# Optimization experiments

Measured on AMD Instinct MI355X. Metric: run time of the kernel, lower is better.

## Reference

```python
import jax, jax.numpy as jnp
import numpy as np

EPS = 1e-12


def conv3(x, W, b):
    # x: [B,C,H,W], W: [O,I,3,3] -> SAME conv, stride 1
    y = jax.lax.conv_general_dilated(x, W, (1, 1), 'SAME',
                                     dimension_numbers=('NCHW', 'OIHW', 'NCHW'))
    return y + b[None, :, None, None]


def unfold3(x):
    # torch F.unfold(kernel=3, padding=1): [B,C,H,W] -> [B, C*9, H*W]
    B, C, H, W = x.shape
    xp = jnp.pad(x, ((0, 0), (0, 0), (1, 1), (1, 1)))
    patches = jnp.stack([xp[:, :, i:i + H, j:j + W]
                         for i in range(3) for j in range(3)], axis=2)  # [B,C,9,H,W]
    return patches.reshape(B, C * 9, H * W)


def fold3(u, H, W):
    # torch F.fold(kernel=3, padding=1): [B, C*9, H*W] -> [B,C,H,W] (overlap-add)
    B = u.shape[0]
    C = u.shape[1] // 9
    p = u.reshape(B, C, 3, 3, H, W)
    out = jnp.zeros((B, C, H + 2, W + 2), u.dtype)
    for i in range(3):
        for j in range(3):
            out = out.at[:, :, i:i + H, j:j + W].add(p[:, :, i, j])
    return out[:, :, 1:-1, 1:-1]


def l2norm(v, axis):
    n = jnp.sqrt(jnp.sum(v * v, axis=axis, keepdims=True))
    return v / jnp.maximum(n, EPS)


def setup_inputs() -> dict:
    key = jax.random.key(0)
    ks = jax.random.split(key, 10)
    in_c, q_c = 64, 32
    B, H, W = 1, 96, 96
    s = 0.05
    return {
        'x':  jax.random.normal(ks[0], (B, in_c, H, W), jnp.float32),
        'W1': jax.random.normal(ks[1], (in_c, in_c, 3, 3), jnp.float32) * s,
        'b1': jax.random.normal(ks[2], (in_c,), jnp.float32) * s,
        'W2': jax.random.normal(ks[3], (in_c, in_c, 3, 3), jnp.float32) * s,
        'b2': jax.random.normal(ks[4], (in_c,), jnp.float32) * s,
        'Wq': jax.random.normal(ks[5], (q_c, in_c, 3, 3), jnp.float32) * s,
        'bq': jax.random.normal(ks[6], (q_c,), jnp.float32) * s,
        'Wk': jax.random.normal(ks[7], (q_c, in_c, 3, 3), jnp.float32) * s,
        'bk': jax.random.normal(ks[8], (q_c,), jnp.float32) * s,
    }


def reference(x, W1, b1, W2, b2, Wq, bq, Wk, bk):
    TOPK = 5
    B, C, H, W = x.shape
    L = H * W

    feature = jax.nn.relu(conv3(jax.nn.relu(conv3(x, W1, b1)), W2, b2))
    q = conv3(x, Wq, bq)
    k = conv3(x, Wk, bk)

    q_unfold = l2norm(unfold3(q), axis=1)                      # [B, Q9, L]
    k_unfold = l2norm(jnp.swapaxes(unfold3(k), 1, 2), axis=2)  # [B, L, Q9]

    R_qk = jnp.einsum('blc,bcm->blm', k_unfold, q_unfold)      # [B, L_k, L_q]

    # topk over dim=1 (key positions) for each query position
    vals, idxs = jax.lax.top_k(jnp.swapaxes(R_qk, 1, 2), TOPK)  # [B, L_q, K]
    R_maxs = jnp.swapaxes(vals, 1, 2)                           # [B, K, L]
    R_indexs = jnp.swapaxes(idxs, 1, 2)                         # [B, K, L]

    x_unfold = unfold3(x)                                       # [B, C*9, L]
    acc = jnp.zeros_like(x)
    for i in range(1, TOPK):
        idx = R_indexs[:, i, :][:, None, :]                     # [B,1,L]
        T_unfold = jnp.take_along_axis(x_unfold, idx, axis=2)   # [B, C*9, L]
        T = fold3(T_unfold, H, W) / 9.0
        S = R_maxs[:, i, :].reshape(B, 1, H, W)
        acc = acc + T * S
    y = feature + x + acc / float(TOPK - 1)
    return y
```

## Files before the change

### kernel.cpp

```cpp
#include <hip/hip_runtime.h>
#include <math.h>

#define HH 96
#define WW 96
#define LL 9216
#define PW 98
#define PCH (PW * PW)
#define D9 288
#define TOPK 5
#define NK 6
#define NCAND 8
#define KSPLIT 32
#define CPQ (KSPLIT * NK)
#define KEYS_PER_SPLIT (LL / KSPLIT)
#define PASSES (KEYS_PER_SPLIT / 32)
#define CHUNKS (32 * 36)
#define KROW 292

typedef short short8 __attribute__((ext_vector_type(8)));
typedef float f32x16 __attribute__((ext_vector_type(16)));

__device__ __forceinline__ float  asf(unsigned u) { union { unsigned u; float f; } a; a.u = u; return a.f; }
__device__ __forceinline__ unsigned asu(float f)  { union { float f; unsigned u; } a; a.f = f; return a.u; }

__device__ __forceinline__ unsigned short f2bf(float f) {
    unsigned u = asu(f);
    unsigned r = u + 0x7fff + ((u >> 16) & 1);
    return (unsigned short)(r >> 16);
}

template<int N>
__device__ __forceinline__ void ins_med3(float* v, float x) {
    float nv[N];
    nv[0] = fmaxf(v[0], x);
    #pragma unroll
    for (int s = 1; s < N; ++s) nv[s] = __builtin_amdgcn_fmed3f(v[s-1], v[s], x);
    #pragma unroll
    for (int s = 0; s < N; ++s) v[s] = nv[s];
}

__device__ __forceinline__ bool better_tb(float av, int ai, float bv, int bi) {
    return (av > bv) || (av == bv && ai < bi);
}

template<int N>
__device__ __forceinline__ void insert_tb(float (&v)[N], int (&ix)[N], float nv, int ni) {
    if (better_tb(nv, ni, v[N-1], ix[N-1])) {
        v[N-1] = nv; ix[N-1] = ni;
        #pragma unroll
        for (int s = N-1; s > 0; --s) {
            if (better_tb(v[s], ix[s], v[s-1], ix[s-1])) {
                float tv = v[s]; v[s] = v[s-1]; v[s-1] = tv;
                int ti = ix[s]; ix[s] = ix[s-1]; ix[s-1] = ti;
            }
        }
    }
}

__global__ __launch_bounds__(256) void pad_init_kernel(
    const float* __restrict__ x, float* __restrict__ xpad, float* __restrict__ c1pad)
{
    int e = blockIdx.x * 256 + threadIdx.x;
    if (blockIdx.y == 1) { c1pad[e] = 0.0f; return; }
    int c = e / PCH, rem = e - c * PCH;
    int r = rem / PW, col = rem - r * PW;
    float val = 0.0f;
    if ((unsigned)(r - 1) < 96u && (unsigned)(col - 1) < 96u)
        val = x[(size_t)c * LL + (r - 1) * WW + (col - 1)];
    xpad[e] = val;
}

template<int NCO>
__device__ __forceinline__ void conv_pipe(
    const float* __restrict__ inpad, const float* __restrict__ Wt,
    const float* __restrict__ bias, int co0,
    float (&acc)[NCO][2])
{
    int t = blockIdx.x * 256 + threadIdx.x;
    int pix0 = t * 2;
    int y = pix0 / WW, x0 = pix0 - y * WW;
    const float* base = inpad + y * PW + x0;

    #pragma unroll
    for (int j = 0; j < NCO; ++j) acc[j][0] = acc[j][1] = bias[co0 + j];

    float2 A[3][2], B[3][2];
    #pragma unroll
    for (int u = 0; u < 3; ++u) {
        A[u][0] = *(const float2*)(base + u * PW);
        A[u][1] = *(const float2*)(base + u * PW + 2);
    }

    #pragma unroll 1
    for (int ci = 0; ci < 64; ci += 2) {
        const float* nb = base + (size_t)(ci + 1) * PCH;
        #pragma unroll
        for (int u = 0; u < 3; ++u) {
            B[u][0] = *(const float2*)(nb + u * PW);
            B[u][1] = *(const float2*)(nb + u * PW + 2);
        }
        {
            const float* wb = Wt + ((size_t)co0 * 64 + ci) * 9;
            #pragma unroll
            for (int j = 0; j < NCO; ++j) {
                const float* wp = wb + (size_t)j * 64 * 9;
                #pragma unroll
                for (int u = 0; u < 3; ++u) {
                    float r0 = A[u][0].x, r1 = A[u][0].y, r2 = A[u][1].x, r3 = A[u][1].y;
                    float w0 = wp[u*3], w1 = wp[u*3+1], w2 = wp[u*3+2];
                    acc[j][0] = fmaf(r0, w0, acc[j][0]);
                    acc[j][1] = fmaf(r1, w0, acc[j][1]);
                    acc[j][0] = fmaf(r1, w1, acc[j][0]);
                    acc[j][1] = fmaf(r2, w1, acc[j][1]);
                    acc[j][0] = fmaf(r2, w2, acc[j][0]);
                    acc[j][1] = fmaf(r3, w2, acc[j][1]);
                }
            }
        }
        if (ci + 2 < 64) {
            const float* nb2 = base + (size_t)(ci + 2) * PCH;
            #pragma unroll
            for (int u = 0; u < 3; ++u) {
                A[u][0] = *(const float2*)(nb2 + u * PW);
                A[u][1] = *(const float2*)(nb2 + u * PW + 2);
            }
        }
        {
            const float* wb = Wt + ((size_t)co0 * 64 + (ci + 1)) * 9;
            #pragma unroll
            for (int j = 0; j < NCO; ++j) {
                const float* wp = wb + (size_t)j * 64 * 9;
                #pragma unroll
                for (int u = 0; u < 3; ++u) {
                    float r0 = B[u][0].x, r1 = B[u][0].y, r2 = B[u][1].x, r3 = B[u][1].y;
                    float w0 = wp[u*3], w1 = wp[u*3+1], w2 = wp[u*3+2];
                    acc[j][0] = fmaf(r0, w0, acc[j][0]);
                    acc[j][1] = fmaf(r1, w0, acc[j][1]);
                    acc[j][0] = fmaf(r1, w1, acc[j][0]);
                    acc[j][1] = fmaf(r2, w1, acc[j][1]);
                    acc[j][0] = fmaf(r2, w2, acc[j][0]);
                    acc[j][1] = fmaf(r3, w2, acc[j][1]);
                }
            }
        }
    }
}

__global__ __launch_bounds__(256) void conv_stage1_kernel(
    const float* __restrict__ xpad,
    const float* __restrict__ W1, const float* __restrict__ b1, float* __restrict__ c1pad,
    const float* __restrict__ Wq, const float* __restrict__ bq,
    const float* __restrict__ Wk, const float* __restrict__ bk,
    float* __restrict__ qq, float* __restrict__ kk)
{
    int g = blockIdx.y;
    int pix0 = (blockIdx.x * 256 + threadIdx.x) * 2;
    int y = pix0 / WW, x0 = pix0 - y * WW;

    if (g < 16) {
        float acc[4][2];
        conv_pipe<4>(xpad, W1, b1, g * 4, acc);
        #pragma unroll
        for (int j = 0; j < 4; ++j) {
            float* o = c1pad + (size_t)(g * 4 + j) * PCH + (y + 1) * PW + (x0 + 1);
            o[0] = fmaxf(acc[j][0], 0.0f);
            o[1] = fmaxf(acc[j][1], 0.0f);
        }
    } else if (g < 24) {
        float acc[4][2];
        conv_pipe<4>(xpad, Wq, bq, (g - 16) * 4, acc);
        #pragma unroll
        for (int j = 0; j < 4; ++j)
            *(float2*)(qq + (size_t)((g - 16) * 4 + j) * LL + pix0) = make_float2(acc[j][0], acc[j][1]);
    } else {
        float acc[4][2];
        conv_pipe<4>(xpad, Wk, bk, (g - 24) * 4, acc);
        #pragma unroll
        for (int j = 0; j < 4; ++j)
            *(float2*)(kk + (size_t)((g - 24) * 4 + j) * LL + pix0) = make_float2(acc[j][0], acc[j][1]);
    }
}

__global__ __launch_bounds__(256) void conv2_kernel(
    const float* __restrict__ c1pad, const float* __restrict__ W2,
    const float* __restrict__ b2, float* __restrict__ feat)
{
    int pix0 = (blockIdx.x * 256 + threadIdx.x) * 2;
    float acc[2][2];
    conv_pipe<2>(c1pad, W2, b2, blockIdx.y * 2, acc);
    #pragma unroll
    for (int j = 0; j < 2; ++j) {
        float2 o;
        o.x = fmaxf(acc[j][0], 0.0f);
        o.y = fmaxf(acc[j][1], 0.0f);
        *(float2*)(feat + (size_t)(blockIdx.y * 2 + j) * LL + pix0) = o;
    }
}

__global__ __launch_bounds__(256) void transpose_x_kernel(
    const float* __restrict__ x, float* __restrict__ xT)
{
    __shared__ float t[64][65];
    int pix0 = blockIdx.x * 64;
    int lp = threadIdx.x & 63, cg = threadIdx.x >> 6;
    #pragma unroll
    for (int cc = 0; cc < 16; ++cc) {
        int c = cg * 16 + cc;
        t[c][lp] = x[(size_t)c * LL + pix0 + lp];
    }
    __syncthreads();
    #pragma unroll
    for (int pp = 0; pp < 16; ++pp) {
        int pl = cg * 16 + pp;
        xT[(size_t)(pix0 + pl) * 64 + lp] = t[lp][pl];
    }
}

__global__ __launch_bounds__(256) void unfold_norm_kernel(
    const float* __restrict__ qq, float* __restrict__ q_f32, unsigned short* __restrict__ q_bf,
    const float* __restrict__ kk, float* __restrict__ k_f32, unsigned short* __restrict__ k_bf)
{
    const float* in; float* o32; unsigned short* obf;
    if (blockIdx.y == 0) { in = qq; o32 = q_f32; obf = q_bf; }
    else                 { in = kk; o32 = k_f32; obf = k_bf; }

    __shared__ float tile[3][32][34];
    __shared__ float inv_s[32];
    int tid = threadIdx.x;
    int l0 = blockIdx.x * 32;
    int y = l0 / WW, xb = l0 % WW;

    #pragma unroll
    for (int j = 0; j < 13; ++j) {
        int f = j * 256 + tid;
        if (f < 3 * 32 * 34) {
            int col = f % 34, cc = (f / 34) & 31, r = f / (34 * 32);
            int yy = y + r - 1, xv = xb + col - 1;
            float val = ((unsigned)yy < 96u && (unsigned)xv < 96u)
                        ? in[(size_t)cc * LL + yy * 96 + xv] : 0.0f;
            tile[r][cc][col] = val;
        }
    }
    __syncthreads();

    {
        int pxl = tid >> 3, sub = tid & 7;
        float ss = 0.0f;
        #pragma unroll
        for (int cc = 0; cc < 4; ++cc) {
            int c = sub * 4 + cc;
            #pragma unroll
            for (int u = 0; u < 3; ++u)
                #pragma unroll
                for (int v = 0; v < 3; ++v) {
                    float val = tile[u][c][pxl + v];
                    ss = fmaf(val, val, ss);
                }
        }
        ss += __shfl_xor(ss, 1);
        ss += __shfl_xor(ss, 2);
        ss += __shfl_xor(ss, 4);
        if (sub == 0) inv_s[pxl] = 1.0f / fmaxf(sqrtf(ss), 1e-12f);
    }
    __syncthreads();

    #pragma unroll 1
    for (int it = 0; it < 9; ++it) {
        int e = it * 256 + tid;
        int pxl = e / 72, dc = e - pxl * 72;
        int l = l0 + pxl;
        float inv = inv_s[pxl];
        float4 o; float* op = &o.x;
        #pragma unroll
        for (int i = 0; i < 4; ++i) {
            int d = dc * 4 + i;
            int c = d / 9, rm = d - c * 9;
            int u = rm / 3, v = rm - u * 3;
            op[i] = tile[u][c][pxl + v] * inv;
        }
        *(float4*)(o32 + (size_t)l * D9 + dc * 4) = o;
        unsigned short b4[4];
        #pragma unroll
        for (int i = 0; i < 4; ++i) b4[i] = f2bf(op[i]);
        *(uint2*)(obf + (size_t)l * D9 + dc * 4) = *(uint2*)b4;
    }
}

__global__ __launch_bounds__(256, 2) void topk_mfma_kernel(
    const unsigned short* __restrict__ qn_bf, const unsigned short* __restrict__ kn_bf,
    float* __restrict__ valsQ)
{
    __shared__ unsigned short ks[2][32 * KROW];

    int tid  = threadIdx.x;
    int lane = tid & 63;
    int col = lane & 31, khalf = lane >> 5;
    int qtile = blockIdx.x >> 5;
    int split = blockIdx.x & 31;
    int q0w = qtile * 256 + (tid >> 6) * 64;
    int key0 = split * KEYS_PER_SPLIT;

    short8 qf[2][18];
    #pragma unroll
    for (int b = 0; b < 2; ++b) {
        const unsigned short* qrow = qn_bf + (size_t)(q0w + b*32 + col) * D9 + khalf * 8;
        #pragma unroll
        for (int dg = 0; dg < 18; ++dg)
            qf[b][dg] = *(const short8*)(qrow + dg * 16);
    }

    float lv0[NK], lv1[NK];
    #pragma unroll
    for (int s = 0; s < NK; ++s) { lv0[s] = -INFINITY; lv1[s] = -INFINITY; }

    const char* kg = (const char*)kn_bf;
    uint4 pre[5];

    #pragma unroll
    for (int c0 = 0; c0 < 5; ++c0) {
        int c = tid + c0 * 256;
        if (c < CHUNKS) {
            int key = c / 36, off = c - key * 36;
            pre[c0] = *(const uint4*)(kg + (size_t)(key0 + key) * 576 + off * 16);
        }
    }
    #pragma unroll
    for (int c0 = 0; c0 < 5; ++c0) {
        int c = tid + c0 * 256;
        if (c < CHUNKS) {
            int key = c / 36, off = c - key * 36;
            char* d = (char*)ks[0] + key * (KROW*2) + off * 16;
            *(uint2*)d       = *(uint2*)&pre[c0];
            *(uint2*)(d + 8) = *((uint2*)&pre[c0] + 1);
        }
    }
    __syncthreads();

    for (int p = 0; p < PASSES; ++p) {
        if (p + 1 < PASSES) {
            #pragma unroll
            for (int c0 = 0; c0 < 5; ++c0) {
                int c = tid + c0 * 256;
                if (c < CHUNKS) {
                    int key = c / 36, off = c - key * 36;
                    pre[c0] = *(const uint4*)(kg + (size_t)(key0 + (p+1)*32 + key) * 576 + off * 16);
                }
            }
        }

        f32x16 acc0 = {}, acc1 = {};
        const char* kb = (const char*)ks[p & 1] + (size_t)col * (KROW*2) + khalf * 16;
        #pragma unroll
        for (int dg = 0; dg < 18; ++dg) {
            short8 af;
            *(uint2*)&af       = *(const uint2*)(kb + dg * 32);
            *((uint2*)&af + 1) = *(const uint2*)(kb + dg * 32 + 8);
            acc0 = __builtin_amdgcn_mfma_f32_32x32x16_bf16(af, qf[0][dg], acc0, 0, 0, 0);
            acc1 = __builtin_amdgcn_mfma_f32_32x32x16_bf16(af, qf[1][dg], acc1, 0, 0, 0);
        }

        int lbase = p * 32 + 4 * khalf;
        #pragma unroll
        for (int r = 0; r < 16; ++r) {
            unsigned lkey = (unsigned)(lbase + (r & 3) + 8 * (r >> 2));
            ins_med3<NK>(lv0, asf((asu(acc0[r]) & 0xFFFFFE00u) | lkey));
            ins_med3<NK>(lv1, asf((asu(acc1[r]) & 0xFFFFFE00u) | lkey));
        }

        if (p + 1 < PASSES) {
            #pragma unroll
            for (int c0 = 0; c0 < 5; ++c0) {
                int c = tid + c0 * 256;
                if (c < CHUNKS) {
                    int key = c / 36, off = c - key * 36;
                    char* d = (char*)ks[(p+1) & 1] + key * (KROW*2) + off * 16;
                    *(uint2*)d       = *(uint2*)&pre[c0];
                    *(uint2*)(d + 8) = *((uint2*)&pre[c0] + 1);
                }
            }
        }
        __syncthreads();
    }

    #pragma unroll
    for (int b = 0; b < 2; ++b) {
        float* lv = b ? lv1 : lv0;
        float pv[NK];
        #pragma unroll
        for (int s = 0; s < NK; ++s) pv[s] = __shfl_xor(lv[s], 32);
        #pragma unroll
        for (int s = 0; s < NK; ++s) ins_med3<NK>(lv, pv[s]);
        if (lane < 32) {
            int q = q0w + b * 32 + col;
            float* vq = valsQ + (size_t)q * CPQ + split * NK;
            #pragma unroll
            for (int s = 0; s < NK; ++s) vq[s] = lv[s];
        }
    }
}

__global__ __launch_bounds__(256) void rerank_kernel(
    const float* __restrict__ valsQ,
    const float* __restrict__ qn_f32, const float* __restrict__ kn_f32,
    float* __restrict__ vals, int* __restrict__ idxs)
{
    int tid = threadIdx.x;
    int lane = tid & 63;
    int half = lane >> 5, l32 = lane & 31;
    int q = blockIdx.x * 8 + (tid >> 6) * 2 + half;

    const float* vq = valsQ + (size_t)q * CPQ + l32 * NK;
    float v[NK];
    #pragma unroll
    for (int s = 0; s < NK; ++s) v[s] = vq[s];

    int ckey[NCAND];
    #pragma unroll
    for (int it = 0; it < NCAND; ++it) {
        float cv = v[0];
        int cl = l32;
        #pragma unroll
        for (int st = 1; st < 32; st <<= 1) {
            float ov = __shfl_xor(cv, st);
            int ol = __shfl_xor(cl, st);
            if (ov > cv || (ov == cv && ol < cl)) { cv = ov; cl = ol; }
        }
        ckey[it] = cl * KEYS_PER_SPLIT + (int)(asu(cv) & 0x1FFu);
        if (cl == l32) {
            #pragma unroll
            for (int s = 0; s < NK-1; ++s) v[s] = v[s+1];
            v[NK-1] = -INFINITY;
        }
    }

    int r = l32 >> 2, part = l32 & 3;
    const float4* qr = (const float4*)(qn_f32 + (size_t)q * D9) + part * 18;
    const float4* kr = (const float4*)(kn_f32 + (size_t)ckey[r] * D9) + part * 18;
    float s0 = 0.f, s1 = 0.f, s2 = 0.f, s3 = 0.f;
    #pragma unroll
    for (int i2 = 0; i2 < 18; ++i2) {
        float4 a = qr[i2], b = kr[i2];
        s0 = fmaf(a.x, b.x, s0); s1 = fmaf(a.y, b.y, s1);
        s2 = fmaf(a.z, b.z, s2); s3 = fmaf(a.w, b.w, s3);
    }
    float sc = (s0 + s1) + (s2 + s3);
    sc += __shfl_xor(sc, 1);
    sc += __shfl_xor(sc, 2);

    float bv[TOPK]; int bi[TOPK];
    #pragma unroll
    for (int s = 0; s < TOPK; ++s) { bv[s] = -INFINITY; bi[s] = 0x7fffffff; }
    #pragma unroll
    for (int cc = 0; cc < NCAND; ++cc) {
        float sv = __shfl(sc, half * 32 + cc * 4);
        insert_tb<TOPK>(bv, bi, sv, ckey[cc]);
    }
    if (l32 == 0) {
        #pragma unroll
        for (int s = 0; s < TOPK; ++s) {
            vals[(size_t)s * LL + q] = bv[s];
            idxs[(size_t)s * LL + q] = bi[s];
        }
    }
}

__global__ __launch_bounds__(256) void gather_out_kernel(
    const float* __restrict__ xT, const float* __restrict__ feat,
    const float* __restrict__ vals, const int* __restrict__ idxs,
    float* __restrict__ out)
{
    int wave = threadIdx.x >> 6, lane = threadIdx.x & 63;
    int pix = blockIdx.x * 4 + wave;
    int y = pix / WW, x0 = pix - y * WW;
    float acc = 0.0f;
    #pragma unroll 1
    for (int s = 1; s < TOPK; ++s) {
        float S = vals[(size_t)s * LL + pix] * (1.0f/9.0f);
        #pragma unroll
        for (int i = 0; i < 3; ++i) {
            int qy = y + 1 - i;
            #pragma unroll
            for (int j = 0; j < 3; ++j) {
                int qx = x0 + 1 - j;
                if ((unsigned)qy < 96u && (unsigned)qx < 96u) {
                    int l = idxs[(size_t)s * LL + qy * WW + qx];
                    int yl = l / WW, xl = l - yl * WW;
                    int sy = yl + i - 1, sx = xl + j - 1;
                    if ((unsigned)sy < 96u && (unsigned)sx < 96u)
                        acc = fmaf(S, xT[(size_t)(sy * WW + sx) * 64 + lane], acc);
                }
            }
        }
    }
    out[(size_t)lane * LL + pix] = feat[(size_t)lane * LL + pix]
                                 + xT[(size_t)pix * 64 + lane] + acc * 0.25f;
}

extern "C" void kernel_launch(void* const* d_in, const int* in_sizes, int n_in,
                              void* d_out, int out_size, void* d_ws, size_t ws_size,
                              hipStream_t stream)
{
    (void)in_sizes; (void)n_in; (void)out_size; (void)ws_size;
    const float* x  = (const float*)d_in[0];
    const float* W1 = (const float*)d_in[1];
    const float* b1 = (const float*)d_in[2];
    const float* W2 = (const float*)d_in[3];
    const float* b2 = (const float*)d_in[4];
    const float* Wq = (const float*)d_in[5];
    const float* bq = (const float*)d_in[6];
    const float* Wk = (const float*)d_in[7];
    const float* bk = (const float*)d_in[8];
    float* out = (float*)d_out;

    char* p = (char*)d_ws;
    float* xpad   = (float*)p;            p += (size_t)64 * PCH * 4;
    float* c1pad  = (float*)p;            p += (size_t)64 * PCH * 4;
    float* feat   = (float*)p;            p += (size_t)64 * LL * 4;
    float* xT     = (float*)p;            p += (size_t)64 * LL * 4;
    float* qq     = (float*)p;            p += (size_t)32 * LL * 4;
    float* kk     = (float*)p;            p += (size_t)32 * LL * 4;
    float* qn_f32 = (float*)p;            p += (size_t)LL * D9 * 4;
    float* kn_f32 = (float*)p;            p += (size_t)LL * D9 * 4;
    unsigned short* qn_bf = (unsigned short*)p;  p += (size_t)LL * D9 * 2;
    unsigned short* kn_bf = (unsigned short*)p;  p += (size_t)LL * D9 * 2;
    float* valsQ  = (float*)p;            p += (size_t)LL * CPQ * 4;
    float* vals   = (float*)p;            p += (size_t)TOPK * LL * 4;
    int*   idxs   = (int*)p;              p += (size_t)TOPK * LL * 4;

    pad_init_kernel<<<dim3(2401, 2), 256, 0, stream>>>(x, xpad, c1pad);
    conv_stage1_kernel<<<dim3(18, 32), 256, 0, stream>>>(xpad, W1, b1, c1pad, Wq, bq, Wk, bk, qq, kk);
    unfold_norm_kernel<<<dim3(288, 2), 256, 0, stream>>>(qq, qn_f32, qn_bf, kk, kn_f32, kn_bf);
    topk_mfma_kernel<<<36 * KSPLIT, 256, 0, stream>>>(qn_bf, kn_bf, valsQ);
    conv2_kernel<<<dim3(18, 32), 256, 0, stream>>>(c1pad, W2, b2, feat);
    transpose_x_kernel<<<144, 256, 0, stream>>>(x, xT);
    rerank_kernel<<<LL / 8, 256, 0, stream>>>(valsQ, qn_f32, kn_f32, vals, idxs);
    gather_out_kernel<<<LL / 4, 256, 0, stream>>>(xT, feat, vals, idxs, out);
}
```

Before: 289.7 us.

## Pre-pack key matrix into MFMA A-fragment layout and drop LDS staging

Adds a repack kernel that lays the bf16 key matrix out in the exact per-lane MFMA A-fragment order. The top-k MFMA kernel then loads fragments straight from global memory (coalesced 16-byte loads) instead of staging keys through double-buffered shared memory with barriers. This removes LDS traffic, the __syncthreads calls and the manual prefetch. In exchange it adds a kernel launch plus an extra pass over the key data. The four waves of a block now read the same key fragments redundantly from global/L2, and there is no explicit software prefetch to hide load latency.

```diff
diff --git a/kernel.cpp b/kernel.cpp
--- a/kernel.cpp
+++ b/kernel.cpp
@@ -14,8 +14,6 @@
 #define CPQ (KSPLIT * NK)
 #define KEYS_PER_SPLIT (LL / KSPLIT)
 #define PASSES (KEYS_PER_SPLIT / 32)
-#define CHUNKS (32 * 36)
-#define KROW 292
 
 typedef short short8 __attribute__((ext_vector_type(8)));
 typedef float f32x16 __attribute__((ext_vector_type(16)));
@@ -286,12 +284,23 @@
     }
 }
 
+__global__ __launch_bounds__(256) void repack_afrag_kernel(
+    const unsigned short* __restrict__ kn_bf, short8* __restrict__ kn_afrag)
+{
+    int flat = blockIdx.x * 256 + threadIdx.x;
+    int lane = flat & 63;
+    int g = flat >> 6;
+    int dg = g % 18;
+    int sp = g / 18;
+    int key = sp * 32 + (lane & 31);
+    int d0 = dg * 16 + (lane >> 5) * 8;
+    kn_afrag[flat] = *(const short8*)(kn_bf + (size_t)key * D9 + d0);
+}
+
 __global__ __launch_bounds__(256, 2) void topk_mfma_kernel(
-    const unsigned short* __restrict__ qn_bf, const unsigned short* __restrict__ kn_bf,
+    const unsigned short* __restrict__ qn_bf, const short8* __restrict__ kn_afrag,
     float* __restrict__ valsQ)
 {
-    __shared__ unsigned short ks[2][32 * KROW];
-
     int tid  = threadIdx.x;
     int lane = tid & 63;
     int col = lane & 31, khalf = lane >> 5;
@@ -313,48 +322,15 @@
     #pragma unroll
     for (int s = 0; s < NK; ++s) { lv0[s] = -INFINITY; lv1[s] = -INFINITY; }
 
-    const char* kg = (const char*)kn_bf;
-    uint4 pre[5];
-
-    #pragma unroll
-    for (int c0 = 0; c0 < 5; ++c0) {
-        int c = tid + c0 * 256;
-        if (c < CHUNKS) {
-            int key = c / 36, off = c - key * 36;
-            pre[c0] = *(const uint4*)(kg + (size_t)(key0 + key) * 576 + off * 16);
-        }
-    }
-    #pragma unroll
-    for (int c0 = 0; c0 < 5; ++c0) {
-        int c = tid + c0 * 256;
-        if (c < CHUNKS) {
-            int key = c / 36, off = c - key * 36;
-            char* d = (char*)ks[0] + key * (KROW*2) + off * 16;
-            *(uint2*)d       = *(uint2*)&pre[c0];
-            *(uint2*)(d + 8) = *((uint2*)&pre[c0] + 1);
-        }
-    }
-    __syncthreads();
-
+    const short8* ka = kn_afrag + (size_t)split * (PASSES * 18 * 64) + lane;
+
+    #pragma unroll 1
     for (int p = 0; p < PASSES; ++p) {
-        if (p + 1 < PASSES) {
-            #pragma unroll
-            for (int c0 = 0; c0 < 5; ++c0) {
-                int c = tid + c0 * 256;
-                if (c < CHUNKS) {
-                    int key = c / 36, off = c - key * 36;
-                    pre[c0] = *(const uint4*)(kg + (size_t)(key0 + (p+1)*32 + key) * 576 + off * 16);
-                }
-            }
-        }
-
+        const short8* kp = ka + p * (18 * 64);
         f32x16 acc0 = {}, acc1 = {};
-        const char* kb = (const char*)ks[p & 1] + (size_t)col * (KROW*2) + khalf * 16;
         #pragma unroll
         for (int dg = 0; dg < 18; ++dg) {
-            short8 af;
-            *(uint2*)&af       = *(const uint2*)(kb + dg * 32);
-            *((uint2*)&af + 1) = *(const uint2*)(kb + dg * 32 + 8);
+            short8 af = kp[dg * 64];
             acc0 = __builtin_amdgcn_mfma_f32_32x32x16_bf16(af, qf[0][dg], acc0, 0, 0, 0);
             acc1 = __builtin_amdgcn_mfma_f32_32x32x16_bf16(af, qf[1][dg], acc1, 0, 0, 0);
         }
@@ -366,20 +342,6 @@
             ins_med3<NK>(lv0, asf((asu(acc0[r]) & 0xFFFFFE00u) | lkey));
             ins_med3<NK>(lv1, asf((asu(acc1[r]) & 0xFFFFFE00u) | lkey));
         }
-
-        if (p + 1 < PASSES) {
-            #pragma unroll
-            for (int c0 = 0; c0 < 5; ++c0) {
-                int c = tid + c0 * 256;
-                if (c < CHUNKS) {
-                    int key = c / 36, off = c - key * 36;
-                    char* d = (char*)ks[(p+1) & 1] + key * (KROW*2) + off * 16;
-                    *(uint2*)d       = *(uint2*)&pre[c0];
-                    *(uint2*)(d + 8) = *((uint2*)&pre[c0] + 1);
-                }
-            }
-        }
-        __syncthreads();
     }
 
     #pragma unroll
@@ -397,6 +359,7 @@
             for (int s = 0; s < NK; ++s) vq[s] = lv[s];
         }
     }
+    (void)key0;
 }
 
 __global__ __launch_bounds__(256) void rerank_kernel(
@@ -523,6 +486,7 @@
     float* kn_f32 = (float*)p;            p += (size_t)LL * D9 * 4;
     unsigned short* qn_bf = (unsigned short*)p;  p += (size_t)LL * D9 * 2;
     unsigned short* kn_bf = (unsigned short*)p;  p += (size_t)LL * D9 * 2;
+    short8* kn_afrag = (short8*)p;        p += (size_t)KSPLIT * PASSES * 18 * 64 * 16;
     float* valsQ  = (float*)p;            p += (size_t)LL * CPQ * 4;
     float* vals   = (float*)p;            p += (size_t)TOPK * LL * 4;
     int*   idxs   = (int*)p;              p += (size_t)TOPK * LL * 4;
@@ -530,7 +494,8 @@
     pad_init_kernel<<<dim3(2401, 2), 256, 0, stream>>>(x, xpad, c1pad);
     conv_stage1_kernel<<<dim3(18, 32), 256, 0, stream>>>(xpad, W1, b1, c1pad, Wq, bq, Wk, bk, qq, kk);
     unfold_norm_kernel<<<dim3(288, 2), 256, 0, stream>>>(qq, qn_f32, qn_bf, kk, kn_f32, kn_bf);
-    topk_mfma_kernel<<<36 * KSPLIT, 256, 0, stream>>>(qn_bf, kn_bf, valsQ);
+    repack_afrag_kernel<<<1296, 256, 0, stream>>>(kn_bf, kn_afrag);
+    topk_mfma_kernel<<<36 * KSPLIT, 256, 0, stream>>>(qn_bf, kn_afrag, valsQ);
     conv2_kernel<<<dim3(18, 32), 256, 0, stream>>>(c1pad, W2, b2, feat);
     transpose_x_kernel<<<144, 256, 0, stream>>>(x, xT);
     rerank_kernel<<<LL / 8, 256, 0, stream>>>(valsQ, qn_f32, kn_f32, vals, idxs);
```

Result: slower. 326.3 us (+12.6%).
